# Kernel optimization log

Hardware: AMD Instinct MI355X
Metric: run time of the kernel (lower is better)

The kernel has to match this reference:

```python
import jax, jax.numpy as jnp
import numpy as np

B, P, D = 64, 128, 128   # clouds, points per cloud, vec_dim
N = B * P                # 8192 nodes
EPS = 1e-5


def _complete_graph_edges():
    # knn_graph with k == total node count => complete graph per cloud (no self loops)
    i = np.arange(P)
    ii, jj = np.meshgrid(i, i, indexing='ij')
    m = ii != jj
    li, lj = ii[m], jj[m]                      # [P*(P-1)] local pairs
    off = (np.arange(B) * P)[:, None]          # cloud offsets
    src = (off + li[None, :]).reshape(-1)      # neighbor index
    dst = (off + lj[None, :]).reshape(-1)      # center index
    return jnp.asarray(src, jnp.int32), jnp.asarray(dst, jnp.int32)


def setup_inputs() -> dict:
    key = jax.random.key(0)
    ks = jax.random.split(key, 4)
    src, dst = _complete_graph_edges()
    return {
        'x': jax.random.normal(ks[0], (N, D), jnp.float32),
        'xyz': jax.random.normal(ks[1], (N, 3), jnp.float32),
        'W_xyz': jax.random.normal(ks[2], (3, D), jnp.float32) * 0.1,
        'bn_gamma': jnp.ones((D,), jnp.float32),
        'bn_beta': jnp.zeros((D,), jnp.float32),
        'W1': jax.random.normal(ks[3], (D, D), jnp.float32) * 0.05,
        'b1': jnp.zeros((D,), jnp.float32),
        'ln_gamma': jnp.ones((D,), jnp.float32),
        'ln_beta': jnp.zeros((D,), jnp.float32),
        'src': src,
        'dst': dst,
    }


def reference(x, xyz, W_xyz, bn_gamma, bn_beta, W1, b1, ln_gamma, ln_beta, src, dst):
    n = x.shape[0]
    rela_xyz = xyz[src] - xyz[dst]                         # [E, 3]
    rela_x = x[src] - x[dst]                               # [E, D]
    dist = jnp.sqrt(jnp.sum(rela_xyz * rela_xyz, axis=-1))  # [E]
    w = jnp.exp(-dist)[:, None]                            # [E, 1]

    # weighted linear + relu, pool by src (global_add_pool over node index)
    h1 = jax.nn.relu((w * rela_x) @ W1 + b1)               # [E, D]
    p1 = jax.ops.segment_sum(h1, src, num_segments=n)      # [N, D]
    mu = jnp.mean(p1, axis=-1, keepdims=True)
    var = jnp.var(p1, axis=-1, keepdims=True)
    x = x + ((p1 - mu) / jnp.sqrt(var + EPS)) * ln_gamma + ln_beta

    # xyz projection branch, BatchNorm1d (training-mode batch stats)
    h2 = jax.nn.relu(rela_xyz @ W_xyz)                     # [E, D]
    p2 = jax.ops.segment_sum(h2, src, num_segments=n)      # [N, D]
    bmu = jnp.mean(p2, axis=0)
    bvar = jnp.var(p2, axis=0)
    x = x + ((p2 - bmu) / jnp.sqrt(bvar + EPS)) * bn_gamma + bn_beta
    return x
```

## Files before the change

### kernel.cpp

```cpp
#include <hip/hip_runtime.h>
#include <stdint.h>

#define EPS 1e-5f
#define N_NODES 8192

typedef __attribute__((ext_vector_type(8))) short short8;
typedef __attribute__((ext_vector_type(4))) float floatx4;

__device__ __forceinline__ short f2bf(float f) {
    uint32_t u = __float_as_uint(f);
    u += 0x7FFFu + ((u >> 16) & 1u);
    return (short)(u >> 16);
}
__device__ __forceinline__ float bf2f(short s) {
    return __uint_as_float(((uint32_t)(uint16_t)s) << 16);
}

__global__ __launch_bounds__(256) void gemm_y_kernel(
    const float* __restrict__ x, const float* __restrict__ W1,
    float* __restrict__ y)
{
    const int wv   = threadIdx.x >> 6;
    const int lane = threadIdx.x & 63;
    const int ml   = lane & 15;
    const int q    = lane >> 4;
    const int rb   = blockIdx.x * 64 + wv * 16;

    short8 afrag[4];
    const float* arow = x + (rb + ml) * 128;
#pragma unroll
    for (int c = 0; c < 4; ++c) {
        const float* ap = arow + c * 32 + q * 8;
        floatx4 lo = *(const floatx4*)ap;
        floatx4 hi = *(const floatx4*)(ap + 4);
        short8 a;
        a[0] = f2bf(lo[0]); a[1] = f2bf(lo[1]); a[2] = f2bf(lo[2]); a[3] = f2bf(lo[3]);
        a[4] = f2bf(hi[0]); a[5] = f2bf(hi[1]); a[6] = f2bf(hi[2]); a[7] = f2bf(hi[3]);
        afrag[c] = a;
    }
#pragma unroll
    for (int nt = 0; nt < 8; ++nt) {
        floatx4 acc = {0.f, 0.f, 0.f, 0.f};
        const int ncol = nt * 16 + ml;
#pragma unroll
        for (int c = 0; c < 4; ++c) {
            const int kb = c * 32 + q * 8;
            short8 b;
#pragma unroll
            for (int j = 0; j < 8; ++j) b[j] = f2bf(W1[(kb + j) * 128 + ncol]);
            acc = __builtin_amdgcn_mfma_f32_16x16x32_bf16(afrag[c], b, acc, 0, 0, 0);
        }
#pragma unroll
        for (int r = 0; r < 4; ++r)
            y[(rb + q * 4 + r) * 128 + ncol] = acc[r];
    }
}

__global__ __launch_bounds__(256) void cloud_main_kernel(
    const float* __restrict__ x, const float* __restrict__ xyz,
    const float* __restrict__ W_xyz, const float* __restrict__ b1,
    const float* __restrict__ ln_gamma, const float* __restrict__ ln_beta,
    const float* __restrict__ y_ws, float* __restrict__ p2_ws,
    float* __restrict__ stat_ws, float* __restrict__ out)
{
    __shared__ float smem[10784];
    short* s_z16 = (short*)smem;
    float* s_w   = smem + 8192;
    float* s_xyz = smem + 10240;
    float* s_mu  = smem + 10752;
    float* s_rs  = smem + 10768;
    float* s_p1  = smem;
    float* s_bn  = smem + 8192;

    const int bx  = blockIdx.x;
    const int c   = bx & 63;
    const int s   = bx >> 6;
    const int tid = threadIdx.x;
    const int d   = tid & 127;
    const int g   = tid >> 7;
    const int node0 = c * 128;

    if (tid < 128) {
        const float* p = xyz + (node0 + tid) * 3;
        s_xyz[tid * 4 + 0] = p[0];
        s_xyz[tid * 4 + 1] = p[1];
        s_xyz[tid * 4 + 2] = p[2];
    }
    __syncthreads();

    {
        float w0 = W_xyz[d], w1 = W_xyz[128 + d], w2 = W_xyz[256 + d];
        for (int jj = 0; jj < 64; ++jj) {
            int j = g * 64 + jj;
            float zv = s_xyz[j * 4] * w0 + s_xyz[j * 4 + 1] * w1 + s_xyz[j * 4 + 2] * w2;
            s_z16[j * 128 + d] = f2bf(zv);
        }
    }
    {
        const int i0 = s * 16;
        for (int e = tid; e < 2048; e += 256) {
            int j = e >> 4, ii = e & 15, ia = i0 + ii;
            float dx = s_xyz[ia * 4]     - s_xyz[j * 4];
            float dy = s_xyz[ia * 4 + 1] - s_xyz[j * 4 + 1];
            float dz = s_xyz[ia * 4 + 2] - s_xyz[j * 4 + 2];
            float dist = sqrtf(dx * dx + dy * dy + dz * dz);
            s_w[j * 16 + ii] = __expf(-dist);
        }
    }
    __syncthreads();

    const int iL0 = s * 16 + g * 8;
    float yi[8], zi[8], acc1[8], acc2[8];
    const float b1d = b1[d];
#pragma unroll
    for (int r = 0; r < 8; ++r) {
        yi[r] = y_ws[(node0 + iL0 + r) * 128 + d];
        zi[r] = bf2f(s_z16[(iL0 + r) * 128 + d]);
        acc1[r] = 0.f; acc2[r] = 0.f;
    }
    const float* yrow = y_ws + node0 * 128 + d;
#pragma unroll 2
    for (int j = 0; j < 128; ++j) {
        float yj = yrow[j * 128];
        float zj = bf2f(s_z16[j * 128 + d]);
        floatx4 w0 = *(const floatx4*)(s_w + j * 16 + g * 8);
        floatx4 w1 = *(const floatx4*)(s_w + j * 16 + g * 8 + 4);
#pragma unroll
        for (int r = 0; r < 8; ++r) {
            float w = (r < 4) ? w0[r] : w1[r - 4];
            float t1 = w * (yi[r] - yj) + b1d;
            acc1[r] += fmaxf(t1, 0.f);
            float t2 = zi[r] - zj;
            acc2[r] += fmaxf(t2, 0.f);
        }
    }
#pragma unroll
    for (int r = 0; r < 8; ++r) acc1[r] -= fmaxf(b1d, 0.f);

    __syncthreads();

    {
        float bs = 0.f, bq = 0.f;
#pragma unroll
        for (int r = 0; r < 8; ++r) {
            s_p1[(g * 8 + r) * 132 + d] = acc1[r];
            bs += acc2[r];
            bq += acc2[r] * acc2[r];
        }
        s_bn[g * 128 + d]       = bs;
        s_bn[256 + g * 128 + d] = bq;
    }
    __syncthreads();

    {
        int ii = tid >> 4, sub = tid & 15;
        float ps = 0.f, pq = 0.f;
#pragma unroll
        for (int e = 0; e < 8; ++e) {
            float v = s_p1[ii * 132 + sub * 8 + e];
            ps += v; pq += v * v;
        }
#pragma unroll
        for (int m = 1; m < 16; m <<= 1) {
            ps += __shfl_xor(ps, m, 64);
            pq += __shfl_xor(pq, m, 64);
        }
        if (sub == 0) {
            float mu  = ps * (1.f / 128.f);
            float var = pq * (1.f / 128.f) - mu * mu;
            s_mu[ii] = mu;
            s_rs[ii] = rsqrtf(var + EPS);
        }
    }
    if (tid < 128) {
        atomicAdd(stat_ws + tid,       s_bn[tid] + s_bn[128 + tid]);
        atomicAdd(stat_ws + 128 + tid, s_bn[256 + tid] + s_bn[384 + tid]);
    }
    __syncthreads();

    const float lng = ln_gamma[d], lnb = ln_beta[d];
#pragma unroll
    for (int r = 0; r < 8; ++r) {
        int ii = g * 8 + r;
        int gi = node0 + iL0 + r;
        float o = x[gi * 128 + d] + (acc1[r] - s_mu[ii]) * s_rs[ii] * lng + lnb;
        out[gi * 128 + d]   = o;
        p2_ws[gi * 128 + d] = acc2[r];
    }
}

__global__ __launch_bounds__(256) void finalize_kernel(
    const float* __restrict__ p2_ws, const float* __restrict__ stat_ws,
    const float* __restrict__ bn_gamma, const float* __restrict__ bn_beta,
    float* __restrict__ out)
{
    int t = blockIdx.x * 256 + threadIdx.x;
    int base = t * 4;
    int d0 = base & 127;
    floatx4 p2 = *(const floatx4*)(p2_ws + base);
    floatx4 o  = *(const floatx4*)(out + base);
#pragma unroll
    for (int e = 0; e < 4; ++e) {
        int dd = d0 + e;
        float mu  = stat_ws[dd] * (1.f / 8192.f);
        float var = stat_ws[128 + dd] * (1.f / 8192.f) - mu * mu;
        float rs  = rsqrtf(var + EPS);
        o[e] += (p2[e] - mu) * rs * bn_gamma[dd] + bn_beta[dd];
    }
    *(floatx4*)(out + base) = o;
}

extern "C" void kernel_launch(void* const* d_in, const int* in_sizes, int n_in,
                              void* d_out, int out_size, void* d_ws, size_t ws_size,
                              hipStream_t stream) {
    const float* x        = (const float*)d_in[0];
    const float* xyz      = (const float*)d_in[1];
    const float* W_xyz    = (const float*)d_in[2];
    const float* bn_gamma = (const float*)d_in[3];
    const float* bn_beta  = (const float*)d_in[4];
    const float* W1       = (const float*)d_in[5];
    const float* b1       = (const float*)d_in[6];
    const float* ln_gamma = (const float*)d_in[7];
    const float* ln_beta  = (const float*)d_in[8];
    float* out = (float*)d_out;

    float* y_ws    = (float*)d_ws;
    float* p2_ws   = y_ws + N_NODES * 128;
    float* stat_ws = p2_ws + N_NODES * 128;

    hipMemsetAsync(stat_ws, 0, 256 * sizeof(float), stream);
    gemm_y_kernel<<<128, 256, 0, stream>>>(x, W1, y_ws);
    cloud_main_kernel<<<512, 256, 0, stream>>>(x, xyz, W_xyz, b1, ln_gamma, ln_beta,
                                               y_ws, p2_ws, stat_ws, out);
    finalize_kernel<<<1024, 256, 0, stream>>>(p2_ws, stat_ws, bn_gamma, bn_beta, out);
}
```

Baseline: 124.7 us.

## Pre-convert GEMM operands, shrink cloud tiles, recompute z on the fly, bank stat atomics

Adds a prep kernel that converts x to bf16, transposes W1 to bf16, and zeroes the stats buffer, replacing the memset. The GEMM now loads vector fragments with one wave per block. The main cloud kernel handles 8 centers per block instead of 16, which doubles the grid. It recomputes the xyz projection per neighbor instead of staging bf16 z in LDS, cutting shared memory to raise occupancy, and packs its math as float2. BN stat atomics are spread over 4 banks, and finalize precomputes per-channel scale and shift in shared memory, at the cost of an extra launch and more y_ws rereads.

```diff
diff --git a/kernel.cpp b/kernel.cpp
--- a/kernel.cpp
+++ b/kernel.cpp
@@ -6,48 +6,60 @@
 
 typedef __attribute__((ext_vector_type(8))) short short8;
 typedef __attribute__((ext_vector_type(4))) float floatx4;
-
-__device__ __forceinline__ short f2bf(float f) {
+typedef __attribute__((ext_vector_type(2))) float floatx2;
+typedef __attribute__((ext_vector_type(4))) unsigned short ushortx4;
+
+__device__ __forceinline__ unsigned short f2bf(float f) {
     uint32_t u = __float_as_uint(f);
     u += 0x7FFFu + ((u >> 16) & 1u);
-    return (short)(u >> 16);
-}
-__device__ __forceinline__ float bf2f(short s) {
-    return __uint_as_float(((uint32_t)(uint16_t)s) << 16);
-}
-
-__global__ __launch_bounds__(256) void gemm_y_kernel(
+    return (unsigned short)(u >> 16);
+}
+
+__global__ __launch_bounds__(256) void prep_kernel(
     const float* __restrict__ x, const float* __restrict__ W1,
+    unsigned short* __restrict__ xb, unsigned short* __restrict__ w1t,
+    float* __restrict__ stat_ws)
+{
+    const int bx = blockIdx.x, tid = threadIdx.x;
+    if (bx < 1024) {
+        const int base = bx * 1024 + tid * 4;
+        floatx4 v = *(const floatx4*)(x + base);
+        ushortx4 o = { f2bf(v[0]), f2bf(v[1]), f2bf(v[2]), f2bf(v[3]) };
+        *(ushortx4*)(xb + base) = o;
+    } else {
+        const int b2 = bx - 1024;
+        const int n = b2 * 8 + (tid >> 5);
+        const int k = (tid & 31) * 4;
+#pragma unroll
+        for (int e = 0; e < 4; ++e)
+            w1t[n * 128 + k + e] = f2bf(W1[(k + e) * 128 + n]);
+        if (b2 == 0) {
+            floatx4 z = {0.f, 0.f, 0.f, 0.f};
+            *(floatx4*)(stat_ws + tid * 4) = z;
+        }
+    }
+}
+
+__global__ __launch_bounds__(64) void gemm_y_kernel(
+    const unsigned short* __restrict__ xb, const unsigned short* __restrict__ w1t,
     float* __restrict__ y)
 {
-    const int wv   = threadIdx.x >> 6;
-    const int lane = threadIdx.x & 63;
-    const int ml   = lane & 15;
-    const int q    = lane >> 4;
-    const int rb   = blockIdx.x * 64 + wv * 16;
+    const int lane = threadIdx.x;
+    const int ml = lane & 15, q = lane >> 4;
+    const int rb = blockIdx.x * 16;
 
     short8 afrag[4];
-    const float* arow = x + (rb + ml) * 128;
-#pragma unroll
-    for (int c = 0; c < 4; ++c) {
-        const float* ap = arow + c * 32 + q * 8;
-        floatx4 lo = *(const floatx4*)ap;
-        floatx4 hi = *(const floatx4*)(ap + 4);
-        short8 a;
-        a[0] = f2bf(lo[0]); a[1] = f2bf(lo[1]); a[2] = f2bf(lo[2]); a[3] = f2bf(lo[3]);
-        a[4] = f2bf(hi[0]); a[5] = f2bf(hi[1]); a[6] = f2bf(hi[2]); a[7] = f2bf(hi[3]);
-        afrag[c] = a;
-    }
+#pragma unroll
+    for (int c = 0; c < 4; ++c)
+        afrag[c] = *(const short8*)(xb + (rb + ml) * 128 + c * 32 + q * 8);
+
 #pragma unroll
     for (int nt = 0; nt < 8; ++nt) {
         floatx4 acc = {0.f, 0.f, 0.f, 0.f};
         const int ncol = nt * 16 + ml;
 #pragma unroll
         for (int c = 0; c < 4; ++c) {
-            const int kb = c * 32 + q * 8;
-            short8 b;
-#pragma unroll
-            for (int j = 0; j < 8; ++j) b[j] = f2bf(W1[(kb + j) * 128 + ncol]);
+            short8 b = *(const short8*)(w1t + ncol * 128 + c * 32 + q * 8);
             acc = __builtin_amdgcn_mfma_f32_16x16x32_bf16(afrag[c], b, acc, 0, 0, 0);
         }
 #pragma unroll
@@ -56,136 +68,132 @@
     }
 }
 
-__global__ __launch_bounds__(256) void cloud_main_kernel(
+__global__ __launch_bounds__(256, 4) void cloud_main_kernel(
     const float* __restrict__ x, const float* __restrict__ xyz,
     const float* __restrict__ W_xyz, const float* __restrict__ b1,
     const float* __restrict__ ln_gamma, const float* __restrict__ ln_beta,
     const float* __restrict__ y_ws, float* __restrict__ p2_ws,
     float* __restrict__ stat_ws, float* __restrict__ out)
 {
-    __shared__ float smem[10784];
-    short* s_z16 = (short*)smem;
-    float* s_w   = smem + 8192;
-    float* s_xyz = smem + 10240;
-    float* s_mu  = smem + 10752;
-    float* s_rs  = smem + 10768;
+    __shared__ float smem[1616];
+    float* s_w   = smem;
+    float* s_xyz = smem + 1024;
     float* s_p1  = smem;
-    float* s_bn  = smem + 8192;
-
-    const int bx  = blockIdx.x;
-    const int c   = bx & 63;
-    const int s   = bx >> 6;
+    float* s_bn  = smem + 1088;
+    float* s_mu  = smem + 1600;
+    float* s_rs  = smem + 1608;
+
+    const int bx = blockIdx.x;
+    const int c = bx & 63, s = bx >> 6;
     const int tid = threadIdx.x;
-    const int d   = tid & 127;
-    const int g   = tid >> 7;
+    const int d = tid & 127, g = tid >> 7;
     const int node0 = c * 128;
+    const int i0 = s * 8;
+    const int iL0 = i0 + g * 4;
 
     if (tid < 128) {
         const float* p = xyz + (node0 + tid) * 3;
         s_xyz[tid * 4 + 0] = p[0];
         s_xyz[tid * 4 + 1] = p[1];
         s_xyz[tid * 4 + 2] = p[2];
-    }
-    __syncthreads();
-
+        s_xyz[tid * 4 + 3] = 0.f;
+    }
+    __syncthreads();
+
+    for (int e = tid; e < 1024; e += 256) {
+        const int j = e >> 3, ii = e & 7, ia = i0 + ii;
+        float dx = s_xyz[ia * 4]     - s_xyz[j * 4];
+        float dy = s_xyz[ia * 4 + 1] - s_xyz[j * 4 + 1];
+        float dz = s_xyz[ia * 4 + 2] - s_xyz[j * 4 + 2];
+        s_w[j * 8 + ii] = __expf(-sqrtf(dx * dx + dy * dy + dz * dz));
+    }
+    __syncthreads();
+
+    const float w0 = W_xyz[d], w1c = W_xyz[128 + d], w2c = W_xyz[256 + d];
+    const float b1d = b1[d];
+
+    floatx2 yi[2], zi[2], a1[2], a2[2];
+#pragma unroll
+    for (int r = 0; r < 4; ++r) {
+        const int ia = iL0 + r;
+        yi[r >> 1][r & 1] = y_ws[(node0 + ia) * 128 + d];
+        zi[r >> 1][r & 1] = s_xyz[ia * 4] * w0 + s_xyz[ia * 4 + 1] * w1c
+                          + s_xyz[ia * 4 + 2] * w2c;
+        a1[r >> 1][r & 1] = 0.f;
+        a2[r >> 1][r & 1] = 0.f;
+    }
+    const floatx2 b1v = {b1d, b1d};
+    const floatx2 zv2 = {0.f, 0.f};
+    const float* yrow = y_ws + node0 * 128 + d;
+
+#pragma unroll 4
+    for (int j = 0; j < 128; ++j) {
+        const float yj = yrow[j * 128];
+        floatx4 xj = *(const floatx4*)(s_xyz + j * 4);
+        const float zj = xj[0] * w0 + xj[1] * w1c + xj[2] * w2c;
+        floatx4 wv = *(const floatx4*)(s_w + j * 8 + g * 4);
+        floatx2 wlo = {wv[0], wv[1]}, whi = {wv[2], wv[3]};
+        floatx2 yj2 = {yj, yj}, zj2 = {zj, zj};
+        floatx2 t0 = wlo * (yi[0] - yj2) + b1v;
+        floatx2 t1 = whi * (yi[1] - yj2) + b1v;
+        a1[0] += __builtin_elementwise_max(t0, zv2);
+        a1[1] += __builtin_elementwise_max(t1, zv2);
+        a2[0] += __builtin_elementwise_max(zi[0] - zj2, zv2);
+        a2[1] += __builtin_elementwise_max(zi[1] - zj2, zv2);
+    }
     {
-        float w0 = W_xyz[d], w1 = W_xyz[128 + d], w2 = W_xyz[256 + d];
-        for (int jj = 0; jj < 64; ++jj) {
-            int j = g * 64 + jj;
-            float zv = s_xyz[j * 4] * w0 + s_xyz[j * 4 + 1] * w1 + s_xyz[j * 4 + 2] * w2;
-            s_z16[j * 128 + d] = f2bf(zv);
-        }
-    }
-    {
-        const int i0 = s * 16;
-        for (int e = tid; e < 2048; e += 256) {
-            int j = e >> 4, ii = e & 15, ia = i0 + ii;
-            float dx = s_xyz[ia * 4]     - s_xyz[j * 4];
-            float dy = s_xyz[ia * 4 + 1] - s_xyz[j * 4 + 1];
-            float dz = s_xyz[ia * 4 + 2] - s_xyz[j * 4 + 2];
-            float dist = sqrtf(dx * dx + dy * dy + dz * dz);
-            s_w[j * 16 + ii] = __expf(-dist);
-        }
-    }
-    __syncthreads();
-
-    const int iL0 = s * 16 + g * 8;
-    float yi[8], zi[8], acc1[8], acc2[8];
-    const float b1d = b1[d];
-#pragma unroll
-    for (int r = 0; r < 8; ++r) {
-        yi[r] = y_ws[(node0 + iL0 + r) * 128 + d];
-        zi[r] = bf2f(s_z16[(iL0 + r) * 128 + d]);
-        acc1[r] = 0.f; acc2[r] = 0.f;
-    }
-    const float* yrow = y_ws + node0 * 128 + d;
-#pragma unroll 2
-    for (int j = 0; j < 128; ++j) {
-        float yj = yrow[j * 128];
-        float zj = bf2f(s_z16[j * 128 + d]);
-        floatx4 w0 = *(const floatx4*)(s_w + j * 16 + g * 8);
-        floatx4 w1 = *(const floatx4*)(s_w + j * 16 + g * 8 + 4);
-#pragma unroll
-        for (int r = 0; r < 8; ++r) {
-            float w = (r < 4) ? w0[r] : w1[r - 4];
-            float t1 = w * (yi[r] - yj) + b1d;
-            acc1[r] += fmaxf(t1, 0.f);
-            float t2 = zi[r] - zj;
-            acc2[r] += fmaxf(t2, 0.f);
-        }
-    }
-#pragma unroll
-    for (int r = 0; r < 8; ++r) acc1[r] -= fmaxf(b1d, 0.f);
-
+        const float sc = fmaxf(b1d, 0.f);
+        floatx2 scv = {sc, sc};
+        a1[0] -= scv; a1[1] -= scv;
+    }
     __syncthreads();
 
     {
         float bs = 0.f, bq = 0.f;
 #pragma unroll
-        for (int r = 0; r < 8; ++r) {
-            s_p1[(g * 8 + r) * 132 + d] = acc1[r];
-            bs += acc2[r];
-            bq += acc2[r] * acc2[r];
-        }
-        s_bn[g * 128 + d]       = bs;
-        s_bn[256 + g * 128 + d] = bq;
+        for (int r = 0; r < 4; ++r) {
+            s_p1[(g * 4 + r) * 136 + d] = a1[r >> 1][r & 1];
+            float v2 = a2[r >> 1][r & 1];
+            bs += v2;
+            bq += v2 * v2;
+        }
+        s_bn[g * 256 + d] = bs;
+        s_bn[g * 256 + 128 + d] = bq;
     }
     __syncthreads();
 
     {
-        int ii = tid >> 4, sub = tid & 15;
-        float ps = 0.f, pq = 0.f;
-#pragma unroll
-        for (int e = 0; e < 8; ++e) {
-            float v = s_p1[ii * 132 + sub * 8 + e];
-            ps += v; pq += v * v;
-        }
-#pragma unroll
-        for (int m = 1; m < 16; m <<= 1) {
+        const int ii = tid >> 5, sub = tid & 31;
+        floatx4 v = *(const floatx4*)(s_p1 + ii * 136 + sub * 4);
+        float ps = v[0] + v[1] + v[2] + v[3];
+        float pq = v[0] * v[0] + v[1] * v[1] + v[2] * v[2] + v[3] * v[3];
+#pragma unroll
+        for (int m = 1; m < 32; m <<= 1) {
             ps += __shfl_xor(ps, m, 64);
             pq += __shfl_xor(pq, m, 64);
         }
         if (sub == 0) {
-            float mu  = ps * (1.f / 128.f);
+            float mu = ps * (1.f / 128.f);
             float var = pq * (1.f / 128.f) - mu * mu;
             s_mu[ii] = mu;
             s_rs[ii] = rsqrtf(var + EPS);
         }
     }
     if (tid < 128) {
-        atomicAdd(stat_ws + tid,       s_bn[tid] + s_bn[128 + tid]);
-        atomicAdd(stat_ws + 128 + tid, s_bn[256 + tid] + s_bn[384 + tid]);
+        const int bank = (s & 3) * 256;
+        atomicAdd(stat_ws + bank + d,       s_bn[d] + s_bn[256 + d]);
+        atomicAdd(stat_ws + bank + 128 + d, s_bn[128 + d] + s_bn[384 + d]);
     }
     __syncthreads();
 
     const float lng = ln_gamma[d], lnb = ln_beta[d];
 #pragma unroll
-    for (int r = 0; r < 8; ++r) {
-        int ii = g * 8 + r;
-        int gi = node0 + iL0 + r;
-        float o = x[gi * 128 + d] + (acc1[r] - s_mu[ii]) * s_rs[ii] * lng + lnb;
-        out[gi * 128 + d]   = o;
-        p2_ws[gi * 128 + d] = acc2[r];
+    for (int r = 0; r < 4; ++r) {
+        const int ii = g * 4 + r;
+        const int gi = node0 + iL0 + r;
+        float o = x[gi * 128 + d] + (a1[r >> 1][r & 1] - s_mu[ii]) * s_rs[ii] * lng + lnb;
+        out[gi * 128 + d] = o;
+        p2_ws[gi * 128 + d] = a2[r >> 1][r & 1];
     }
 }
 
@@ -194,19 +202,30 @@
     const float* __restrict__ bn_gamma, const float* __restrict__ bn_beta,
     float* __restrict__ out)
 {
-    int t = blockIdx.x * 256 + threadIdx.x;
-    int base = t * 4;
-    int d0 = base & 127;
+    __shared__ float sA[128], sB[128];
+    const int tid = threadIdx.x;
+    if (tid < 128) {
+        float sm = 0.f, sq = 0.f;
+#pragma unroll
+        for (int b = 0; b < 4; ++b) {
+            sm += stat_ws[b * 256 + tid];
+            sq += stat_ws[b * 256 + 128 + tid];
+        }
+        float mu = sm * (1.f / 8192.f);
+        float var = sq * (1.f / 8192.f) - mu * mu;
+        float rs = rsqrtf(var + EPS);
+        float A = rs * bn_gamma[tid];
+        sA[tid] = A;
+        sB[tid] = bn_beta[tid] - mu * A;
+    }
+    __syncthreads();
+    const int base = (blockIdx.x * 256 + tid) * 4;
+    const int d0 = base & 127;
     floatx4 p2 = *(const floatx4*)(p2_ws + base);
     floatx4 o  = *(const floatx4*)(out + base);
 #pragma unroll
-    for (int e = 0; e < 4; ++e) {
-        int dd = d0 + e;
-        float mu  = stat_ws[dd] * (1.f / 8192.f);
-        float var = stat_ws[128 + dd] * (1.f / 8192.f) - mu * mu;
-        float rs  = rsqrtf(var + EPS);
-        o[e] += (p2[e] - mu) * rs * bn_gamma[dd] + bn_beta[dd];
-    }
+    for (int e = 0; e < 4; ++e)
+        o[e] += p2[e] * sA[d0 + e] + sB[d0 + e];
     *(floatx4*)(out + base) = o;
 }
 
@@ -227,10 +246,12 @@
     float* y_ws    = (float*)d_ws;
     float* p2_ws   = y_ws + N_NODES * 128;
     float* stat_ws = p2_ws + N_NODES * 128;
-
-    hipMemsetAsync(stat_ws, 0, 256 * sizeof(float), stream);
-    gemm_y_kernel<<<128, 256, 0, stream>>>(x, W1, y_ws);
-    cloud_main_kernel<<<512, 256, 0, stream>>>(x, xyz, W_xyz, b1, ln_gamma, ln_beta,
-                                               y_ws, p2_ws, stat_ws, out);
+    unsigned short* xb  = (unsigned short*)(stat_ws + 1024);
+    unsigned short* w1t = xb + N_NODES * 128;
+
+    prep_kernel<<<1040, 256, 0, stream>>>(x, W1, xb, w1t, stat_ws);
+    gemm_y_kernel<<<512, 64, 0, stream>>>(xb, w1t, y_ws);
+    cloud_main_kernel<<<1024, 256, 0, stream>>>(x, xyz, W_xyz, b1, ln_gamma, ln_beta,
+                                                y_ws, p2_ws, stat_ws, out);
     finalize_kernel<<<1024, 256, 0, stream>>>(p2_ws, stat_ws, bn_gamma, bn_beta, out);
 }
```

Measured after the change: 118.3 us. 1.05x faster.
